# Kernel tuning notes

Measured on AMD Instinct MI355X. Metric: run time of the kernel, lower is better.

## Reference

```python
import jax, jax.numpy as jnp
import numpy as np

N = 1_000_000
D_IN = 128
D_OUT = 128
S = 8192  # num_samples


def setup_inputs() -> dict:
    key = jax.random.key(0)
    k1, k2, k3, k4 = jax.random.split(key, 4)
    element_embeddings = jax.random.normal(k1, (N, D_IN), dtype=jnp.float32)
    w_att = jax.random.normal(k2, (D_IN,), dtype=jnp.float32) * (1.0 / np.sqrt(D_IN))
    w_out = jax.random.normal(k3, (D_OUT, D_IN), dtype=jnp.float32) * (1.0 / np.sqrt(D_IN))
    element_to_sample_map = jax.random.randint(k4, (N,), 0, S, dtype=jnp.int32)
    return {
        "element_embeddings": element_embeddings,
        "w_att": w_att,
        "w_out": w_out,
        "element_to_sample_map": element_to_sample_map,
        "num_samples": S,
    }


def reference(element_embeddings, w_att, w_out, element_to_sample_map, num_samples):
    idx = element_to_sample_map
    # attention scores: Linear(D_in, 1, bias=False) -> [N]
    scores = element_embeddings @ w_att  # [N]
    # scatter log-softmax over segments (eps=0), numerically stable
    seg_max = jax.ops.segment_max(scores, idx, num_segments=num_samples)  # [S]
    shifted = scores - seg_max[idx]  # [N]
    seg_sumexp = jax.ops.segment_sum(jnp.exp(shifted), idx, num_segments=num_samples)  # [S]
    attention_probs = jnp.exp(shifted - jnp.log(seg_sumexp)[idx])  # [N]
    # output projection then weighted scatter-sum pooling
    projected = element_embeddings @ w_out.T  # [N, D_out]
    return jax.ops.segment_sum(projected * attention_probs[:, None], idx, num_segments=num_samples)  # [S, D_out]
```

## Files before the change

kernel.cpp:

```cpp
#include <hip/hip_runtime.h>
#include <math.h>

__global__ __launch_bounds__(256) void k_hist(const int* __restrict__ idx,
                                              int* __restrict__ counts, int n) {
    int i = blockIdx.x * 256 + threadIdx.x;
    if (i < n) atomicAdd(&counts[idx[i]], 1);
}

__global__ __launch_bounds__(1024) void k_scan(const int* __restrict__ counts,
                                               int* __restrict__ base,
                                               int* __restrict__ cursor, int S) {
    __shared__ int sh[1024];
    int t = threadIdx.x;
    int loc[8];
    int sum = 0;
#pragma unroll
    for (int j = 0; j < 8; ++j) {
        int g = t * 8 + j;
        loc[j] = sum;
        sum += (g < S) ? counts[g] : 0;
    }
    sh[t] = sum;
    __syncthreads();
    int total = sum;
    for (int off = 1; off < 1024; off <<= 1) {
        int v = (t >= off) ? sh[t - off] : 0;
        __syncthreads();
        sh[t] += v;
        __syncthreads();
    }
    int excl = sh[t] - total;
#pragma unroll
    for (int j = 0; j < 8; ++j) {
        int g = t * 8 + j;
        if (g < S) {
            int b = excl + loc[j];
            base[g] = b;
            cursor[g] = b;
        }
    }
}

__global__ __launch_bounds__(256) void k_scatter(const int* __restrict__ idx,
                                                 int* __restrict__ cursor,
                                                 int* __restrict__ order, int n) {
    int i = blockIdx.x * 256 + threadIdx.x;
    if (i < n) {
        int s = idx[i];
        int pos = atomicAdd(&cursor[s], 1);
        order[pos] = i;
    }
}

__global__ __launch_bounds__(256, 8) void k_pool(
        const float* __restrict__ emb, const float* __restrict__ w_att,
        const int* __restrict__ base, const int* __restrict__ counts,
        const int* __restrict__ order, float* __restrict__ pooled, int S) {
    int wave = (blockIdx.x << 2) | (threadIdx.x >> 6);
    int lane = threadIdx.x & 63;
    if (wave >= S) return;
    int b   = base[wave];
    int cnt = counts[wave];
    int half = lane >> 5;
    int l32  = lane & 31;
    float4 wa = *reinterpret_cast<const float4*>(w_att + 4 * l32);
    float4 acc = make_float4(0.f, 0.f, 0.f, 0.f);
    float Z = 0.f;
    for (int e = 0; e < cnt; e += 2) {
        int sub = e + half;
        bool valid = sub < cnt;
        int sidx = valid ? sub : (cnt - 1);
        int i = order[b + sidx];
        const float4 v = *reinterpret_cast<const float4*>(emb + (size_t)i * 128 + 4 * l32);
        float part = v.x * wa.x + v.y * wa.y + v.z * wa.z + v.w * wa.w;
#pragma unroll
        for (int m = 1; m < 32; m <<= 1) part += __shfl_xor(part, m, 64);
        float ex = valid ? __expf(part) : 0.f;
        Z += ex;
        acc.x = fmaf(ex, v.x, acc.x);
        acc.y = fmaf(ex, v.y, acc.y);
        acc.z = fmaf(ex, v.z, acc.z);
        acc.w = fmaf(ex, v.w, acc.w);
    }
    acc.x += __shfl_xor(acc.x, 32, 64);
    acc.y += __shfl_xor(acc.y, 32, 64);
    acc.z += __shfl_xor(acc.z, 32, 64);
    acc.w += __shfl_xor(acc.w, 32, 64);
    Z     += __shfl_xor(Z,     32, 64);
    float rn = (cnt > 0) ? (1.0f / Z) : 0.f;
    if (half == 0) {
        float4 o = make_float4(acc.x * rn, acc.y * rn, acc.z * rn, acc.w * rn);
        *reinterpret_cast<float4*>(pooled + (size_t)wave * 128 + 4 * l32) = o;
    }
}

#define SPB 8
__global__ __launch_bounds__(256, 4) void k_proj(
        const float* __restrict__ w_out, float* __restrict__ io, int S) {
    __shared__ float wl[128][68];
    __shared__ float pl[2][64];
    int t = threadIdx.x;
    int d = t & 127;
    int h = t >> 7;
    int s0 = blockIdx.x * SPB;
    float acc[SPB / 2];
#pragma unroll
    for (int j = 0; j < SPB / 2; ++j) acc[j] = 0.f;

    for (int ph = 0; ph < 2; ++ph) {
        __syncthreads();
        for (int j = t; j < 2048; j += 256) {
            int r  = j >> 4;
            int c4 = j & 15;
            float4 wv = reinterpret_cast<const float4*>(w_out + (size_t)r * 128 + ph * 64)[c4];
            wl[r][c4 * 4 + 0] = wv.x;
            wl[r][c4 * 4 + 1] = wv.y;
            wl[r][c4 * 4 + 2] = wv.z;
            wl[r][c4 * 4 + 3] = wv.w;
        }
        __syncthreads();
#pragma unroll
        for (int g = 0; g < SPB; g += 2) {
            if (t < 128) {
                int hh = t >> 6, kk = t & 63;
                int ss = s0 + g + hh;
                pl[hh][kk] = (ss < S) ? io[(size_t)ss * 128 + ph * 64 + kk] : 0.f;
            }
            __syncthreads();
            float a = 0.f;
#pragma unroll
            for (int k4 = 0; k4 < 16; ++k4) {
                float4 wv = *reinterpret_cast<const float4*>(&wl[d][k4 * 4]);
                float4 pv = *reinterpret_cast<const float4*>(&pl[h][k4 * 4]);
                a = fmaf(wv.x, pv.x, a);
                a = fmaf(wv.y, pv.y, a);
                a = fmaf(wv.z, pv.z, a);
                a = fmaf(wv.w, pv.w, a);
            }
            acc[g >> 1] += a;
            __syncthreads();
        }
    }
#pragma unroll
    for (int g = 0; g < SPB; g += 2) {
        int s = s0 + g + h;
        if (s < S) io[(size_t)s * 128 + d] = acc[g >> 1];
    }
}

extern "C" void kernel_launch(void* const* d_in, const int* in_sizes, int n_in,
                              void* d_out, int out_size, void* d_ws, size_t ws_size,
                              hipStream_t stream) {
    const float* emb   = (const float*)d_in[0];
    const float* w_att = (const float*)d_in[1];
    const float* w_out = (const float*)d_in[2];
    const int*   idx   = (const int*)d_in[3];
    const int N = in_sizes[0] / 128;
    const int S = out_size / 128;

    char* ws = (char*)d_ws;
    int* counts = (int*)(ws + 0);
    int* base   = (int*)(ws + 32 * 1024);
    int* cursor = (int*)(ws + 64 * 1024);
    int* order  = (int*)(ws + 128 * 1024);
    float* out  = (float*)d_out;

    hipMemsetAsync(counts, 0, (size_t)S * sizeof(int), stream);
    k_hist   <<<(N + 255) / 256, 256, 0, stream>>>(idx, counts, N);
    k_scan   <<<1, 1024, 0, stream>>>(counts, base, cursor, S);
    k_scatter<<<(N + 255) / 256, 256, 0, stream>>>(idx, cursor, order, N);
    k_pool   <<<(S + 3) / 4, 256, 0, stream>>>(emb, w_att, base, counts, order, out, S);
    k_proj   <<<(S + SPB - 1) / SPB, 256, 0, stream>>>(w_out, out, S);
}
```

Before: 279.5 us.

## Process four rows per wave with software-prefetched gathers in pooling kernel

The pooling kernel now splits each wave into four 16-lane groups, so each group handles one embedding row using two float4 loads per lane, and each iteration covers four elements instead of two. The next row's index and data are loaded before the current row is processed, overlapping gather latency with the dot product, exp and accumulation. This shortens the shuffle reduction per element but adds more live registers, so the launch-bounds occupancy hint drops from 8 to 4. It also does one redundant prefetch past the end of each segment.

Result: faster. 261.8 us (-6.3%).

```diff
diff --git a/kernel.cpp b/kernel.cpp
--- a/kernel.cpp
+++ b/kernel.cpp
@@ -52,45 +52,76 @@
     }
 }
 
-__global__ __launch_bounds__(256, 8) void k_pool(
+__global__ __launch_bounds__(256, 4) void k_pool(
         const float* __restrict__ emb, const float* __restrict__ w_att,
         const int* __restrict__ base, const int* __restrict__ counts,
         const int* __restrict__ order, float* __restrict__ pooled, int S) {
     int wave = (blockIdx.x << 2) | (threadIdx.x >> 6);
     int lane = threadIdx.x & 63;
     if (wave >= S) return;
+    int g   = lane >> 4;
+    int l16 = lane & 15;
     int b   = base[wave];
     int cnt = counts[wave];
-    int half = lane >> 5;
-    int l32  = lane & 31;
-    float4 wa = *reinterpret_cast<const float4*>(w_att + 4 * l32);
-    float4 acc = make_float4(0.f, 0.f, 0.f, 0.f);
+    const float* wrow = w_att + 8 * l16;
+    float4 wa0 = *reinterpret_cast<const float4*>(wrow);
+    float4 wa1 = *reinterpret_cast<const float4*>(wrow + 4);
+    float4 a0 = make_float4(0.f, 0.f, 0.f, 0.f);
+    float4 a1 = make_float4(0.f, 0.f, 0.f, 0.f);
     float Z = 0.f;
-    for (int e = 0; e < cnt; e += 2) {
-        int sub = e + half;
-        bool valid = sub < cnt;
-        int sidx = valid ? sub : (cnt - 1);
-        int i = order[b + sidx];
-        const float4 v = *reinterpret_cast<const float4*>(emb + (size_t)i * 128 + 4 * l32);
-        float part = v.x * wa.x + v.y * wa.y + v.z * wa.z + v.w * wa.w;
-#pragma unroll
-        for (int m = 1; m < 32; m <<= 1) part += __shfl_xor(part, m, 64);
-        float ex = valid ? __expf(part) : 0.f;
-        Z += ex;
-        acc.x = fmaf(ex, v.x, acc.x);
-        acc.y = fmaf(ex, v.y, acc.y);
-        acc.z = fmaf(ex, v.z, acc.z);
-        acc.w = fmaf(ex, v.w, acc.w);
-    }
-    acc.x += __shfl_xor(acc.x, 32, 64);
-    acc.y += __shfl_xor(acc.y, 32, 64);
-    acc.z += __shfl_xor(acc.z, 32, 64);
-    acc.w += __shfl_xor(acc.w, 32, 64);
-    Z     += __shfl_xor(Z,     32, 64);
-    float rn = (cnt > 0) ? (1.0f / Z) : 0.f;
-    if (half == 0) {
-        float4 o = make_float4(acc.x * rn, acc.y * rn, acc.z * rn, acc.w * rn);
-        *reinterpret_cast<float4*>(pooled + (size_t)wave * 128 + 4 * l32) = o;
+    if (cnt > 0) {
+        int nit = (cnt + 3) >> 2;
+        int e = g;
+        int i0 = order[b + (e < cnt ? e : cnt - 1)];
+        const float* r = emb + (size_t)i0 * 128 + 8 * l16;
+        float4 v0 = *reinterpret_cast<const float4*>(r);
+        float4 v1 = *reinterpret_cast<const float4*>(r + 4);
+        for (int it = 0; it < nit; ++it) {
+            int en = e + 4;
+            int inext = order[b + (en < cnt ? en : cnt - 1)];
+            const float* rn = emb + (size_t)inext * 128 + 8 * l16;
+            float4 n0 = *reinterpret_cast<const float4*>(rn);
+            float4 n1 = *reinterpret_cast<const float4*>(rn + 4);
+            float part = v0.x * wa0.x + v0.y * wa0.y + v0.z * wa0.z + v0.w * wa0.w
+                       + v1.x * wa1.x + v1.y * wa1.y + v1.z * wa1.z + v1.w * wa1.w;
+            part += __shfl_xor(part, 1);
+            part += __shfl_xor(part, 2);
+            part += __shfl_xor(part, 4);
+            part += __shfl_xor(part, 8);
+            float ex = (e < cnt) ? __expf(part) : 0.f;
+            Z += ex;
+            a0.x = fmaf(ex, v0.x, a0.x);
+            a0.y = fmaf(ex, v0.y, a0.y);
+            a0.z = fmaf(ex, v0.z, a0.z);
+            a0.w = fmaf(ex, v0.w, a0.w);
+            a1.x = fmaf(ex, v1.x, a1.x);
+            a1.y = fmaf(ex, v1.y, a1.y);
+            a1.z = fmaf(ex, v1.z, a1.z);
+            a1.w = fmaf(ex, v1.w, a1.w);
+            v0 = n0;
+            v1 = n1;
+            e = en;
+        }
+    }
+#pragma unroll
+    for (int m = 16; m <= 32; m <<= 1) {
+        a0.x += __shfl_xor(a0.x, m);
+        a0.y += __shfl_xor(a0.y, m);
+        a0.z += __shfl_xor(a0.z, m);
+        a0.w += __shfl_xor(a0.w, m);
+        a1.x += __shfl_xor(a1.x, m);
+        a1.y += __shfl_xor(a1.y, m);
+        a1.z += __shfl_xor(a1.z, m);
+        a1.w += __shfl_xor(a1.w, m);
+        Z    += __shfl_xor(Z,    m);
+    }
+    float rn_ = (Z > 0.f) ? (1.0f / Z) : 0.f;
+    if (g == 0) {
+        float* o = pooled + (size_t)wave * 128 + 8 * l16;
+        float4 o0 = make_float4(a0.x * rn_, a0.y * rn_, a0.z * rn_, a0.w * rn_);
+        float4 o1 = make_float4(a1.x * rn_, a1.y * rn_, a1.z * rn_, a1.w * rn_);
+        *reinterpret_cast<float4*>(o)     = o0;
+        *reinterpret_cast<float4*>(o + 4) = o1;
     }
 }
 
```
